# Kernel optimization log

Measured on AMD Instinct MI355X. Metric: run time of the kernel, lower is better.

The kernel has to match this reference:

```python
import jax, jax.numpy as jnp
import numpy as np
import math

H = 16          # n_heads
D = 1024        # hidden_dim
HD = D // H     # head_dim = 64
LR = 256        # Linformer low-rank length L
MAX_T = 4096    # max_seq_len


def setup_inputs() -> dict:
    key = jax.random.key(0)
    ks = jax.random.split(key, 7)
    X = jax.random.normal(ks[0], (4, 4096, D), dtype=jnp.float32)
    # lecun_normal ~ N(0, 1/fan_in)
    W_kernel = jax.random.normal(ks[1], (D, 3 * D), dtype=jnp.float32) / math.sqrt(D)
    W_bias = jnp.zeros((3 * D,), dtype=jnp.float32)
    low_rank_E = jax.random.normal(ks[2], (MAX_T, H, LR), dtype=jnp.float32) / math.sqrt(MAX_T)
    low_rank_V = jax.random.normal(ks[3], (MAX_T, H, LR), dtype=jnp.float32) / math.sqrt(MAX_T)
    o_kernel = jax.random.normal(ks[4], (D, D), dtype=jnp.float32) / math.sqrt(D)
    o_bias = jnp.zeros((D,), dtype=jnp.float32)
    return {"X": X, "W_kernel": W_kernel, "W_bias": W_bias,
            "low_rank_E": low_rank_E, "low_rank_V": low_rank_V,
            "o_kernel": o_kernel, "o_bias": o_bias}


def reference(X, W_kernel, W_bias, low_rank_E, low_rank_V, o_kernel, o_bias):
    B, T, _ = X.shape
    # L2-normalize tokens
    norm = jnp.linalg.norm(X, ord=2, axis=-1, keepdims=True)  # (B,T,1)
    Xn = X / norm
    # fused QKV projection
    qkv = Xn @ W_kernel + W_bias                 # (B,T,3D)
    qkv = qkv.reshape(B, T, 3, H, HD)
    Q, K, V = qkv[:, :, 0], qkv[:, :, 1], qkv[:, :, 2]   # (B,T,H,HD)
    # low-rank sequence projection of K/V: T -> L
    E = low_rank_E[:T]                            # (T,H,L)
    F = low_rank_V[:T]                            # (T,H,L)
    Kp = jnp.einsum('THK,BTHD->BHKD', E, K)       # (B,H,L,HD)
    Vp = jnp.einsum('THK,BTHD->BHKD', F, V)       # (B,H,L,HD)
    Qh = Q.transpose(0, 2, 1, 3)                  # (B,H,T,HD)
    logits = jnp.einsum('BHTD,BHKD->BHTK', Qh, Kp) / math.sqrt(HD)
    attn = jax.nn.softmax(logits, axis=-1)        # (B,H,T,L)
    out = jnp.einsum('BHTK,BHKD->BHTD', attn, Vp) # (B,H,T,HD)
    out = out.transpose(0, 2, 1, 3).reshape(B, T, H * HD)
    return out @ o_kernel + o_bias
```

## Files before the change

kernel.cpp:

```cpp
#include <hip/hip_runtime.h>
#include <stdint.h>

typedef unsigned short u16;
typedef uint32_t u32;
typedef __bf16 bf16x8 __attribute__((ext_vector_type(8)));
typedef float f32x4 __attribute__((ext_vector_type(4)));

__device__ __forceinline__ u16 f2bf(float f) {
    u32 u = __builtin_bit_cast(u32, f);
    u += 0x7fffu + ((u >> 16) & 1u);
    return (u16)(u >> 16);
}

__device__ __forceinline__ f32x4 mfma16(bf16x8 a, bf16x8 b, f32x4 c) {
    return __builtin_amdgcn_mfma_f32_16x16x32_bf16(a, b, c, 0, 0, 0);
}

__device__ __forceinline__ void gld_lds16(void* lds, const void* g) {
    __builtin_amdgcn_global_load_lds(
        (__attribute__((address_space(1))) void*)(uintptr_t)g,
        (__attribute__((address_space(3))) void*)(u32)(uintptr_t)lds,
        16, 0, 0);
}

__global__ __launch_bounds__(256) void k_prep(
    const float* __restrict__ X, u16* __restrict__ Xn,
    const float* __restrict__ Wk, u16* __restrict__ Wt,
    const float* __restrict__ Ok, u16* __restrict__ Ot,
    const float* __restrict__ E, u16* __restrict__ Et,
    const float* __restrict__ F, u16* __restrict__ Ft) {
    __shared__ float tile[64][65];
    const int tid = threadIdx.x;
    int bid = blockIdx.x;

    if (bid < 16384) {
        const int row = bid;
        const float4 v = ((const float4*)(X + (size_t)row * 1024))[tid];
        float ss = v.x * v.x + v.y * v.y + v.z * v.z + v.w * v.w;
#pragma unroll
        for (int m = 1; m < 64; m <<= 1) ss += __shfl_xor(ss, m);
        if ((tid & 63) == 0) tile[0][tid >> 6] = ss;
        __syncthreads();
        const float sc = 1.0f / sqrtf(tile[0][0] + tile[0][1] + tile[0][2] + tile[0][3]);
        ushort4 o;
        o.x = f2bf(v.x * sc); o.y = f2bf(v.y * sc);
        o.z = f2bf(v.z * sc); o.w = f2bf(v.w * sc);
        ((ushort4*)(Xn + (size_t)row * 1024))[tid] = o;
        return;
    }
    bid -= 16384;
    const float* src; u16* dst; int R, rstride, c0, r0;
    if (bid < 768) {
        src = Wk; dst = Wt; R = 1024; rstride = 3072;
        c0 = (bid % 48) * 64; r0 = (bid / 48) * 64;
    } else if (bid < 1024) {
        const int t = bid - 768;
        src = Ok; dst = Ot; R = 1024; rstride = 1024;
        c0 = (t & 15) * 64; r0 = (t >> 4) * 64;
    } else if (bid < 5120) {
        const int t = bid - 1024;
        const int x = t & 3, y = (t >> 2) & 63, z = t >> 8;
        src = E + (size_t)z * 256; dst = Et + (size_t)z * 1048576;
        R = 4096; rstride = 4096;
        c0 = x * 64; r0 = y * 64;
    } else {
        const int t = bid - 5120;
        const int x = t & 3, y = (t >> 2) & 63, z = t >> 8;
        src = F + (size_t)z * 256; dst = Ft + (size_t)z * 1048576;
        R = 4096; rstride = 4096;
        c0 = x * 64; r0 = y * 64;
    }
    const int lr = tid >> 4, lc = tid & 15;
#pragma unroll
    for (int i = 0; i < 4; ++i) {
        const int r = lr + 16 * i;
        const float4 v = *(const float4*)(src + (size_t)(r0 + r) * rstride + c0 + lc * 4);
        tile[r][lc * 4 + 0] = v.x; tile[r][lc * 4 + 1] = v.y;
        tile[r][lc * 4 + 2] = v.z; tile[r][lc * 4 + 3] = v.w;
    }
    __syncthreads();
    const int c = tid >> 2, seg = tid & 3;
    u32 w[8];
#pragma unroll
    for (int j = 0; j < 8; ++j) {
        const u32 lo = f2bf(tile[seg * 16 + 2 * j][c]);
        const u32 hi = f2bf(tile[seg * 16 + 2 * j + 1][c]);
        w[j] = lo | (hi << 16);
    }
    u16* dp = dst + (size_t)(c0 + c) * R + r0 + seg * 16;
    uint4 q0; q0.x = w[0]; q0.y = w[1]; q0.z = w[2]; q0.w = w[3];
    uint4 q1; q1.x = w[4]; q1.y = w[5]; q1.z = w[6]; q1.w = w[7];
    *(uint4*)dp = q0;
    *((uint4*)dp + 1) = q1;
}

#define G8_PRE(Aptr, Bptr)                                                       \
    const int tid = threadIdx.x, lane = tid & 63;                                \
    const int wid = tid >> 6, wm = wid >> 2, wn = wid & 3;                       \
    const int cl = lane & 15, g = lane >> 4;                                     \
    const int colb = (tid & 7) * 16;                                             \
    const int scb = colb ^ (((tid >> 3) & 7) << 4);                              \
    const int rbA = ((tid >> 3) & 31) + ((tid >> 8) << 7);                       \
    const int rbB = tid >> 3;                                                    \
    const char* gA = (const char*)(Aptr) + (size_t)(m0 + rbA) * 2048 + scb;      \
    const char* gB = (const char*)(Bptr) + (size_t)(n0 + rbB) * 2048 + scb;      \
    const u32 lA = (u32)(rbA * 128 + colb);                                      \
    const u32 lB = (u32)(65536 + rbB * 128 + colb);                              \
    const int xr0 = (g * 16) ^ ((cl & 7) << 4);                                  \
    const int xr1 = (64 + g * 16) ^ ((cl & 7) << 4);

#define G8_STA(q, tau, beta) gld_lds16(sm + (beta) + lA + (q) * 4096,            \
                                       gA + (q) * 65536 + (size_t)(tau) * 128);
#define G8_STB(c, tau, beta) gld_lds16(sm + (beta) + lB + (c) * 8192,            \
                                       gB + (c) * 131072 + (size_t)(tau) * 128);

#define G8_RDB(beta)                                                             \
    _Pragma("unroll") for (int nf = 0; nf < 4; ++nf) {                           \
        const u32 rb_ = (beta) + 65536 + (u32)(wn * 64 + nf * 16 + cl) * 128;    \
        bF[nf][0] = *(const bf16x8*)(sm + rb_ + xr0);                            \
        bF[nf][1] = *(const bf16x8*)(sm + rb_ + xr1);                            \
    }
#define G8_RDA2(dst, q, beta)                                                    \
    _Pragma("unroll") for (int m = 0; m < 2; ++m) {                              \
        const u32 ra_ = (beta) + (u32)(wm * 128 + (q) * 32 + m * 16 + cl) * 128; \
        dst[m][0] = *(const bf16x8*)(sm + ra_ + xr0);                            \
        dst[m][1] = *(const bf16x8*)(sm + ra_ + xr1);                            \
    }

#define G8_WAIT4 asm volatile("s_waitcnt lgkmcnt(4)" ::: "memory");              \
    __builtin_amdgcn_sched_barrier(0);
#define G8_WAIT0 asm volatile("s_waitcnt lgkmcnt(0)" ::: "memory");              \
    __builtin_amdgcn_sched_barrier(0);

#define G8_MMA(q, SRC)                                                           \
    __builtin_amdgcn_s_setprio(1);                                               \
    _Pragma("unroll") for (int m = 0; m < 2; ++m)                                \
        _Pragma("unroll") for (int nf = 0; nf < 4; ++nf) {                       \
            acc[(q)*2 + m][nf] = mfma16(SRC[m][0], bF[nf][0], acc[(q)*2 + m][nf]);\
            acc[(q)*2 + m][nf] = mfma16(SRC[m][1], bF[nf][1], acc[(q)*2 + m][nf]);\
        }                                                                        \
    __builtin_amdgcn_s_setprio(0);                                               \
    __builtin_amdgcn_s_barrier();                                                \
    __builtin_amdgcn_sched_barrier(0);

#define G8_LOOP                                                                  \
    bf16x8 aFe[2][2], aFo[2][2], bF[4][2];                                       \
    G8_STA(0, 0, 0) G8_STB(0, 0, 0) G8_STA(1, 0, 0) G8_STB(1, 0, 0)              \
    G8_STA(2, 0, 0) G8_STB(2, 0, 0) G8_STA(3, 0, 0) G8_STB(3, 0, 0)              \
    G8_STA(0, 1, 32768) G8_STB(0, 1, 32768)                                      \
    G8_STA(1, 1, 32768) G8_STB(1, 1, 32768)                                      \
    G8_STA(2, 1, 32768) G8_STB(2, 1, 32768)                                      \
    for (int it = 0; it < 8; ++it) {                                             \
        const int t1 = 2 * it + 1, t2v = 2 * it + 2, t3v = 2 * it + 3;           \
        const bool nt = (it < 7);                                                \
                                                                         \
        G8_STA(3, t1, 32768) G8_STB(3, t1, 32768)                                \
        asm volatile("s_waitcnt vmcnt(8)" ::: "memory");                         \
        __builtin_amdgcn_s_barrier();                                            \
        G8_RDB(0) G8_RDA2(aFe, 0, 0) G8_RDA2(aFo, 1, 0)                          \
        G8_WAIT4 G8_MMA(0, aFe)                                                  \
                                                                         \
        if (nt) { G8_STA(0, t2v, 0) G8_STB(0, t2v, 0) }                          \
        G8_RDA2(aFe, 2, 0)                                                       \
        G8_WAIT4 G8_MMA(1, aFo)                                                  \
                                                                         \
        if (nt) { G8_STA(1, t2v, 0) G8_STB(1, t2v, 0) }                          \
        G8_RDA2(aFo, 3, 0)                                                       \
        G8_WAIT4 G8_MMA(2, aFe)                                                  \
                                                                         \
        if (nt) { G8_STA(2, t2v, 0) G8_STB(2, t2v, 0) }                          \
        G8_WAIT0 G8_MMA(3, aFo)                                                  \
                                                                         \
        if (nt) {                                                                \
            G8_STA(3, t2v, 0) G8_STB(3, t2v, 0)                                  \
            asm volatile("s_waitcnt vmcnt(8)" ::: "memory");                     \
        } else {                                                                 \
            asm volatile("s_waitcnt vmcnt(0)" ::: "memory");                     \
        }                                                                        \
        __builtin_amdgcn_s_barrier();                                            \
        G8_RDB(32768) G8_RDA2(aFe, 0, 32768) G8_RDA2(aFo, 1, 32768)              \
        G8_WAIT4 G8_MMA(0, aFe)                                                  \
                                                                         \
        if (nt) { G8_STA(0, t3v, 32768) G8_STB(0, t3v, 32768) }                  \
        G8_RDA2(aFe, 2, 32768)                                                   \
        G8_WAIT4 G8_MMA(1, aFo)                                                  \
                                                                         \
        if (nt) { G8_STA(1, t3v, 32768) G8_STB(1, t3v, 32768) }                  \
        G8_RDA2(aFo, 3, 32768)                                                   \
        G8_WAIT4 G8_MMA(2, aFe)                                                  \
                                                                         \
        if (nt) { G8_STA(2, t3v, 32768) G8_STB(2, t3v, 32768) }                  \
        G8_WAIT0 G8_MMA(3, aFo)                                                  \
    }

__global__ __launch_bounds__(512, 2) void k_gemm_qkv(
    const u16* __restrict__ A, const u16* __restrict__ Bt,
    const float* __restrict__ bias,
    u16* __restrict__ Qo, u16* __restrict__ Kt, u16* __restrict__ Vt) {
    __shared__ __align__(16) char sm[131072];
    u32 bid = blockIdx.x;
    bid = (bid & 7) * 96 + (bid >> 3);
    const int m0 = (int)(bid / 12) * 256, n0 = (int)(bid % 12) * 256;

    G8_PRE(A, Bt)

    const f32x4 fz = {0.f, 0.f, 0.f, 0.f};
    f32x4 acc[8][4];
#pragma unroll
    for (int i = 0; i < 8; ++i)
#pragma unroll
        for (int j = 0; j < 4; ++j) acc[i][j] = fz;

    G8_LOOP

    const int segb = n0 >> 10;
    if (segb == 0) {
#pragma unroll
        for (int mf = 0; mf < 8; ++mf) {
            const int mbase = m0 + wm * 128 + mf * 16 + g * 4;
#pragma unroll
            for (int nf = 0; nf < 4; ++nf) {
                const int n = n0 + wn * 64 + nf * 16 + cl;
                const float bv = bias[n];
                f32x4 v = acc[mf][nf];
#pragma unroll
                for (int r = 0; r < 4; ++r)
                    Qo[(size_t)(mbase + r) * 1024 + n] = f2bf(v[r] + bv);
            }
        }
    } else {
        u16* dst = (segb == 1) ? Kt : Vt;
        const int hd0 = n0 & 1023;
#pragma unroll
        for (int mf = 0; mf < 8; ++mf) {
            const int mbase = m0 + wm * 128 + mf * 16 + g * 4;
            const int b = mbase >> 12;
            const int t = mbase & 4095;
#pragma unroll
            for (int nf = 0; nf < 4; ++nf) {
                const int nl = wn * 64 + nf * 16 + cl;
                const float bv = bias[n0 + nl];
                const int hd = hd0 + nl;
                f32x4 v = acc[mf][nf];
                ushort4 pk;
                pk.x = f2bf(v[0] + bv); pk.y = f2bf(v[1] + bv);
                pk.z = f2bf(v[2] + bv); pk.w = f2bf(v[3] + bv);
                *(ushort4*)(dst + (size_t)(b * 1024 + hd) * 4096 + t) = pk;
            }
        }
    }
}

__global__ __launch_bounds__(512, 2) void k_gemm_out(
    const u16* __restrict__ A, const u16* __restrict__ Bt,
    const float* __restrict__ bias, float* __restrict__ out) {
    __shared__ __align__(16) char sm[131072];
    u32 bid = blockIdx.x;
    bid = (bid & 7) * 32 + (bid >> 3);
    const int m0 = (int)(bid / 4) * 256, n0 = (int)(bid % 4) * 256;

    G8_PRE(A, Bt)

    const f32x4 fz = {0.f, 0.f, 0.f, 0.f};
    f32x4 acc[8][4];
#pragma unroll
    for (int i = 0; i < 8; ++i)
#pragma unroll
        for (int j = 0; j < 4; ++j) acc[i][j] = fz;

    G8_LOOP

#pragma unroll
    for (int mf = 0; mf < 8; ++mf) {
        const int mbase = m0 + wm * 128 + mf * 16 + g * 4;
#pragma unroll
        for (int nf = 0; nf < 4; ++nf) {
            const int n = n0 + wn * 64 + nf * 16 + cl;
            const float bv = bias[n];
            f32x4 v = acc[mf][nf];
#pragma unroll
            for (int r = 0; r < 4; ++r)
                out[(size_t)(mbase + r) * 1024 + n] = v[r] + bv;
        }
    }
}

__global__ __launch_bounds__(512) void k_gemm_kpvp(
    const u16* __restrict__ Et, const u16* __restrict__ Ft,
    const u16* __restrict__ Kt, const u16* __restrict__ Vt,
    float* __restrict__ Pp) {
    __shared__ __align__(16) char sm[49152];
    const int tid = threadIdx.x, lane = tid & 63, wid = tid >> 6;
    const int wm = wid >> 2, wn = wid & 3;
    const int cl = lane & 15, g = lane >> 4;
    const int mT = blockIdx.x;
    const int hs = blockIdx.y;
    const int h = hs & 15, s = hs >> 4;
    const int ks = blockIdx.z;

    const int rA = tid >> 2, c16 = tid & 3;
    const int scol = (c16 ^ ((rA >> 1) & 3)) * 8;
    const u16 *gA, *gB0, *gB1;
    if (s == 0) {
        gA = Et + (size_t)h * (256 * 4096) + (size_t)(mT * 128 + rA) * 4096
             + ks * 1024 + scol;
        gB0 = Kt + (size_t)((((rA >> 6) * 16 + h) * 64) + (rA & 63)) * 4096
              + ks * 1024 + scol;
        const int rB1 = rA + 128;
        gB1 = Kt + (size_t)((((rB1 >> 6) * 16 + h) * 64) + (rB1 & 63)) * 4096
              + ks * 1024 + scol;
    } else {
        const int dc = mT * 128 + rA;
        gA = Vt + (size_t)(((dc >> 6) * 16 + h) * 64 + (dc & 63)) * 4096
             + ks * 1024 + scol;
        gB0 = Ft + (size_t)h * (256 * 4096) + (size_t)rA * 4096 + ks * 1024 + scol;
        gB1 = gB0 + (size_t)128 * 4096;
    }
    const u32 lA = (u32)(rA * 64 + c16 * 16);
    const u32 lB0 = (u32)(8192 + rA * 64 + c16 * 16);
    const u32 lB1 = lB0 + 128 * 64;
    const int xsw = (g ^ ((cl >> 1) & 3)) * 16;

    const f32x4 fz = {0.f, 0.f, 0.f, 0.f};
    f32x4 acc[4][4];
#pragma unroll
    for (int i = 0; i < 4; ++i)
#pragma unroll
        for (int j = 0; j < 4; ++j) acc[i][j] = fz;

    gld_lds16(sm + lA, gA); gld_lds16(sm + lB0, gB0); gld_lds16(sm + lB1, gB1);

    u32 roff = 0;
    for (int kt = 0; kt < 32; ++kt) {
        const u32 woff = roff ^ 24576;
        if (kt < 31) {
            gld_lds16(sm + woff + lA, gA + (kt + 1) * 32);
            gld_lds16(sm + woff + lB0, gB0 + (kt + 1) * 32);
            gld_lds16(sm + woff + lB1, gB1 + (kt + 1) * 32);
            asm volatile("s_waitcnt vmcnt(3)" ::: "memory");
        } else {
            asm volatile("s_waitcnt vmcnt(0)" ::: "memory");
        }
        __builtin_amdgcn_s_barrier();
        __builtin_amdgcn_sched_barrier(0);
        const char* rb = sm + roff;
        bf16x8 aF[4], bF[4];
#pragma unroll
        for (int mf = 0; mf < 4; ++mf)
            aF[mf] = *(const bf16x8*)(rb + (wm * 64 + mf * 16 + cl) * 64 + xsw);
#pragma unroll
        for (int nf = 0; nf < 4; ++nf)
            bF[nf] = *(const bf16x8*)(rb + 8192 + (wn * 64 + nf * 16 + cl) * 64 + xsw);
        asm volatile("s_waitcnt lgkmcnt(0)" ::: "memory");
        __builtin_amdgcn_sched_barrier(0);
        __builtin_amdgcn_s_setprio(1);
#pragma unroll
        for (int mf = 0; mf < 4; ++mf)
#pragma unroll
            for (int nf = 0; nf < 4; ++nf)
                acc[mf][nf] = mfma16(aF[mf], bF[nf], acc[mf][nf]);
        __builtin_amdgcn_s_setprio(0);
        asm volatile("s_waitcnt lgkmcnt(0)" ::: "memory");
        __builtin_amdgcn_s_barrier();
        roff = woff;
    }

    float* P = Pp + ((size_t)(ks * 32 + hs) << 16);
#pragma unroll
    for (int mf = 0; mf < 4; ++mf) {
        const int m = mT * 128 + wm * 64 + mf * 16 + g * 4;
#pragma unroll
        for (int nf = 0; nf < 4; ++nf) {
            const int nn = wn * 64 + nf * 16 + cl;
            f32x4 v = acc[mf][nf];
#pragma unroll
            for (int r = 0; r < 4; ++r)
                P[(size_t)(m + r) * 256 + nn] = v[r];
        }
    }
}

__global__ __launch_bounds__(256) void k_red(const float* __restrict__ Pp,
                                             u16* __restrict__ Kp,
                                             u16* __restrict__ Vpt) {
    const int e = blockIdx.x * 256 + threadIdx.x;
    const int hs = e >> 14;
    const int rem = (e & 16383) * 4;
    float4 sum = {0.f, 0.f, 0.f, 0.f};
#pragma unroll
    for (int ks = 0; ks < 4; ++ks) {
        const float4 v = *(const float4*)(Pp + (((size_t)(ks * 32 + hs)) << 16) + rem);
        sum.x += v.x; sum.y += v.y; sum.z += v.z; sum.w += v.w;
    }
    const int m = rem >> 8, col = rem & 255;
    const int h = hs & 15, sf = hs >> 4;
    ushort4 pk;
    pk.x = f2bf(sum.x); pk.y = f2bf(sum.y);
    pk.z = f2bf(sum.z); pk.w = f2bf(sum.w);
    if (sf == 0) {
        const int bh = (col >> 6) * 16 + h, d0 = col & 63;
        *(ushort4*)(Kp + (size_t)bh * 16384 + m * 64 + d0) = pk;
    } else {
        const int bh = (m >> 6) * 16 + h, d = m & 63;
        *(ushort4*)(Vpt + (size_t)bh * 16384 + d * 256 + col) = pk;
    }
}

__global__ __launch_bounds__(256, 1) void k_attn(
    const u16* __restrict__ Q, const u16* __restrict__ Kp,
    const u16* __restrict__ Vpt, u16* __restrict__ AO) {
    __shared__ __align__(16) char sm[65536];
    const int lane = threadIdx.x & 63, wid = threadIdx.x >> 6;
    const int cl = lane & 15, g = lane >> 4;
    const int tT = blockIdx.x, h = blockIdx.y, b = blockIdx.z;
    const int bh = b * 16 + h;
    const int trow0 = b * 4096 + tT * 128 + wid * 32;
    const u16* Qb = Q + (size_t)trow0 * 1024 + h * 64;
    const u16* KpB = Kp + (size_t)bh * (256 * 64);
    const u16* VpB = Vpt + (size_t)bh * (64 * 256);
    char* sP = sm + wid * 16384;

    bf16x8 qF[2][2];
#pragma unroll
    for (int nf = 0; nf < 2; ++nf)
#pragma unroll
        for (int ks = 0; ks < 2; ++ks)
            qF[nf][ks] = *(const bf16x8*)(Qb + (size_t)(nf * 16 + cl) * 1024 + ks * 32 + g * 8);

    const f32x4 fz = {0.f, 0.f, 0.f, 0.f};
    f32x4 Sp[16][2];
#pragma unroll
    for (int mf = 0; mf < 16; ++mf) { Sp[mf][0] = fz; Sp[mf][1] = fz; }

#pragma unroll
    for (int mf = 0; mf < 16; ++mf) {
#pragma unroll
        for (int ks = 0; ks < 2; ++ks) {
            bf16x8 aF = *(const bf16x8*)(KpB + (size_t)(mf * 16 + cl) * 64 + ks * 32 + g * 8);
            Sp[mf][0] = mfma16(aF, qF[0][ks], Sp[mf][0]);
            Sp[mf][1] = mfma16(aF, qF[1][ks], Sp[mf][1]);
        }
    }

    float inv_sum[2];
#pragma unroll
    for (int nf = 0; nf < 2; ++nf) {
        float mx = -1e30f;
#pragma unroll
        for (int mf = 0; mf < 16; ++mf)
#pragma unroll
            for (int r = 0; r < 4; ++r) {
                float x = Sp[mf][nf][r] * 0.125f;
                Sp[mf][nf][r] = x;
                mx = fmaxf(mx, x);
            }
        mx = fmaxf(mx, __shfl_xor(mx, 16));
        mx = fmaxf(mx, __shfl_xor(mx, 32));
        float sum = 0.f;
#pragma unroll
        for (int mf = 0; mf < 16; ++mf)
#pragma unroll
            for (int r = 0; r < 4; ++r) {
                float p = __expf(Sp[mf][nf][r] - mx);
                Sp[mf][nf][r] = p;
                sum += p;
            }
        sum += __shfl_xor(sum, 16);
        sum += __shfl_xor(sum, 32);
        inv_sum[nf] = 1.0f / sum;

        const int tl = nf * 16 + cl;
        const int sw = (tl & 7) << 4;
#pragma unroll
        for (int mf = 0; mf < 16; ++mf) {
            uint2 pk;
            pk.x = (u32)f2bf(Sp[mf][nf][0]) | ((u32)f2bf(Sp[mf][nf][1]) << 16);
            pk.y = (u32)f2bf(Sp[mf][nf][2]) | ((u32)f2bf(Sp[mf][nf][3]) << 16);
            *(uint2*)(sP + ((tl * 512 + (mf * 16 + g * 4) * 2) ^ sw)) = pk;
        }
    }

    f32x4 Oa[4][2];
#pragma unroll
    for (int mf = 0; mf < 4; ++mf) { Oa[mf][0] = fz; Oa[mf][1] = fz; }
#pragma unroll
    for (int ks = 0; ks < 8; ++ks) {
        bf16x8 aF[4];
#pragma unroll
        for (int mf = 0; mf < 4; ++mf)
            aF[mf] = *(const bf16x8*)(VpB + (size_t)(mf * 16 + cl) * 256 + ks * 32 + g * 8);
#pragma unroll
        for (int nf = 0; nf < 2; ++nf) {
            const int tl = nf * 16 + cl;
            const int sw = (tl & 7) << 4;
            bf16x8 bF = *(const bf16x8*)(sP + ((tl * 512 + (ks * 32 + g * 8) * 2) ^ sw));
#pragma unroll
            for (int mf = 0; mf < 4; ++mf)
                Oa[mf][nf] = mfma16(aF[mf], bF, Oa[mf][nf]);
        }
    }

#pragma unroll
    for (int nf = 0; nf < 2; ++nf) {
        const int t = trow0 + nf * 16 + cl;
#pragma unroll
        for (int mf = 0; mf < 4; ++mf) {
            f32x4 v = Oa[mf][nf];
            ushort4 pk;
            pk.x = f2bf(v[0] * inv_sum[nf]); pk.y = f2bf(v[1] * inv_sum[nf]);
            pk.z = f2bf(v[2] * inv_sum[nf]); pk.w = f2bf(v[3] * inv_sum[nf]);
            *(ushort4*)(AO + (size_t)t * 1024 + h * 64 + mf * 16 + g * 4) = pk;
        }
    }
}

extern "C" void kernel_launch(void* const* d_in, const int* in_sizes, int n_in,
                              void* d_out, int out_size, void* d_ws, size_t ws_size,
                              hipStream_t stream) {
    const float* X  = (const float*)d_in[0];
    const float* Wk = (const float*)d_in[1];
    const float* Wb = (const float*)d_in[2];
    const float* E  = (const float*)d_in[3];
    const float* F  = (const float*)d_in[4];
    const float* Ok = (const float*)d_in[5];
    const float* Ob = (const float*)d_in[6];
    float* out = (float*)d_out;
    char* ws = (char*)d_ws;

    u16* Xn  = (u16*)(ws + 0);
    u16* Wt  = (u16*)(ws + 33554432);
    u16* Ot  = (u16*)(ws + 39845888);
    u16* Et  = (u16*)(ws + 41943040);
    u16* Ft  = (u16*)(ws + 75497472);
    u16* Qb  = (u16*)(ws + 109051904);
    u16* Kt  = (u16*)(ws + 142606336);
    u16* Vt  = (u16*)(ws + 176160768);
    u16* Kp  = (u16*)(ws + 209715200);
    u16* Vpt = (u16*)(ws + 211812352);
    float* Pp = (float*)(ws + 0);
    u16* AO  = Xn;

    k_prep<<<25600, 256, 0, stream>>>(X, Xn, Wk, Wt, Ok, Ot, E, Et, F, Ft);
    k_gemm_qkv<<<768, 512, 0, stream>>>(Xn, Wt, Wb, Qb, Kt, Vt);
    k_gemm_kpvp<<<dim3(2, 32, 4), 512, 0, stream>>>(Et, Ft, Kt, Vt, Pp);
    k_red<<<2048, 256, 0, stream>>>(Pp, Kp, Vpt);
    k_attn<<<dim3(32, 16, 4), 256, 0, stream>>>(Qb, Kp, Vpt, AO);
    k_gemm_out<<<256, 512, 0, stream>>>(AO, Ot, Ob, out);
}
```

Before: 338.5 us.

## Deepen K/V projection pipeline to four LDS stages and remap QKV block tiles per XCD

The K/V low-rank projection kernel moves from a double-buffered LDS pipeline to a four-stage ring with three tiles prefetched ahead, using graded vmcnt waits. This hides more global-load latency behind the MFMA loop. The cost is doubling LDS to 96KB per block, which can cut occupancy. The QKV GEMM also changes its block-to-tile mapping so each XCD owns a contiguous group of M rows, aiming for better L2 reuse of A.

```diff
diff --git a/kernel.cpp b/kernel.cpp
--- a/kernel.cpp
+++ b/kernel.cpp
@@ -198,9 +198,9 @@
     const float* __restrict__ bias,
     u16* __restrict__ Qo, u16* __restrict__ Kt, u16* __restrict__ Vt) {
     __shared__ __align__(16) char sm[131072];
-    u32 bid = blockIdx.x;
-    bid = (bid & 7) * 96 + (bid >> 3);
-    const int m0 = (int)(bid / 12) * 256, n0 = (int)(bid % 12) * 256;
+    const u32 raw = blockIdx.x;
+    const int xcd = (int)(raw & 7), cid = (int)(raw >> 3);
+    const int m0 = (xcd * 8 + (cid & 7)) * 256, n0 = (cid >> 3) * 256;
 
     G8_PRE(A, Bt)
 
@@ -289,7 +289,7 @@
     const u16* __restrict__ Et, const u16* __restrict__ Ft,
     const u16* __restrict__ Kt, const u16* __restrict__ Vt,
     float* __restrict__ Pp) {
-    __shared__ __align__(16) char sm[49152];
+    __shared__ __align__(16) char sm[98304];
     const int tid = threadIdx.x, lane = tid & 63, wid = tid >> 6;
     const int wm = wid >> 2, wn = wid & 3;
     const int cl = lane & 15, g = lane >> 4;
@@ -328,22 +328,29 @@
 #pragma unroll
         for (int j = 0; j < 4; ++j) acc[i][j] = fz;
 
-    gld_lds16(sm + lA, gA); gld_lds16(sm + lB0, gB0); gld_lds16(sm + lB1, gB1);
-
-    u32 roff = 0;
+#define KP_STAGE(kt)                                                             \
+    {                                                                            \
+        const u32 bo = ((kt) & 3) * 24576;                                       \
+        gld_lds16(sm + bo + lA,  gA + (kt) * 32);                                \
+        gld_lds16(sm + bo + lB0, gB0 + (kt) * 32);                               \
+        gld_lds16(sm + bo + lB1, gB1 + (kt) * 32);                               \
+    }
+    KP_STAGE(0) KP_STAGE(1) KP_STAGE(2)
+
     for (int kt = 0; kt < 32; ++kt) {
-        const u32 woff = roff ^ 24576;
-        if (kt < 31) {
-            gld_lds16(sm + woff + lA, gA + (kt + 1) * 32);
-            gld_lds16(sm + woff + lB0, gB0 + (kt + 1) * 32);
-            gld_lds16(sm + woff + lB1, gB1 + (kt + 1) * 32);
+        if (kt < 29) {
+            KP_STAGE(kt + 3)
+            asm volatile("s_waitcnt vmcnt(9)" ::: "memory");
+        } else if (kt == 29) {
+            asm volatile("s_waitcnt vmcnt(6)" ::: "memory");
+        } else if (kt == 30) {
             asm volatile("s_waitcnt vmcnt(3)" ::: "memory");
         } else {
             asm volatile("s_waitcnt vmcnt(0)" ::: "memory");
         }
         __builtin_amdgcn_s_barrier();
         __builtin_amdgcn_sched_barrier(0);
-        const char* rb = sm + roff;
+        const char* rb = sm + (kt & 3) * 24576;
         bf16x8 aF[4], bF[4];
 #pragma unroll
         for (int mf = 0; mf < 4; ++mf)
@@ -360,10 +367,10 @@
             for (int nf = 0; nf < 4; ++nf)
                 acc[mf][nf] = mfma16(aF[mf], bF[nf], acc[mf][nf]);
         __builtin_amdgcn_s_setprio(0);
-        asm volatile("s_waitcnt lgkmcnt(0)" ::: "memory");
         __builtin_amdgcn_s_barrier();
-        roff = woff;
-    }
+        __builtin_amdgcn_sched_barrier(0);
+    }
+#undef KP_STAGE
 
     float* P = Pp + ((size_t)(ks * 32 + hs) << 16);
 #pragma unroll
```

Measured after the change: 343.5 us. Within noise of the previous version (+1.5%).
